# Optimization experiments

Measured on AMD Instinct MI355X. Metric: run time of the kernel, lower is better.

Reference implementation:

```python
import jax, jax.numpy as jnp
import numpy as np

B, L, D = 8192, 2048, 256


def setup_inputs() -> dict:
    key = jax.random.key(0)
    kx, kl = jax.random.split(key)
    x = jax.random.normal(kx, (B, D), dtype=jnp.float32)
    landmarks = jax.random.normal(kl, (L, D), dtype=jnp.float32)
    return {"x": x, "landmarks": landmarks}


def reference(x, landmarks):
    # RBF layer: out[b, l] = exp(-gamma * sum_d (landmarks[l, d] - x[b, d])^2)
    # gamma='auto' -> 1 / n_features (landmarks.shape[1])
    gamma = jnp.float32(1.0 / landmarks.shape[1])
    # avoids materializing the [B, L, D] broadcast-diff intermediate)
    x2 = jnp.sum(x * x, axis=-1, keepdims=True)          # [B, 1]
    l2 = jnp.sum(landmarks * landmarks, axis=-1)         # [L]
    cross = jnp.einsum('bd,ld->bl', x, landmarks)        # [B, L]
    d2 = jnp.maximum(x2 + l2[None, :] - 2.0 * cross, 0.0)
    return jnp.exp(-gamma * d2)
```

## Files before the change

kernel.cpp:

```cpp
#include <hip/hip_runtime.h>


typedef __bf16 bf16x8 __attribute__((ext_vector_type(8)));
typedef float  f32x4  __attribute__((ext_vector_type(4)));

#define B_ROWS 8192
#define L_ROWS 2048
#define K_DIM  256

#define GLD_LDS(g, l) __builtin_amdgcn_global_load_lds(                      \
    (const __attribute__((address_space(1))) void*)(g),                      \
    (__attribute__((address_space(3))) void*)(l), 16, 0, 0)

__device__ __forceinline__ unsigned short f32_to_bf16_rne(float f) {
    union { float f; unsigned int u; } v; v.f = f;
    unsigned int u = v.u;
    unsigned int r = (u + 0x7fffu + ((u >> 16) & 1u)) >> 16;
    return (unsigned short)r;
}

__global__ __launch_bounds__(256) void cvt_rows_kernel(
    const float* __restrict__ in, unsigned short* __restrict__ outb,
    float* __restrict__ sq)
{
    const int lane = threadIdx.x & 63;
    const int row  = blockIdx.x * 4 + (threadIdx.x >> 6);
    const float4 v = ((const float4*)(in + row * K_DIM))[lane];
    ushort4 o;
    o.x = f32_to_bf16_rne(v.x);
    o.y = f32_to_bf16_rne(v.y);
    o.z = f32_to_bf16_rne(v.z);
    o.w = f32_to_bf16_rne(v.w);
    ((ushort4*)(outb + row * K_DIM))[lane] = o;
    float s = v.x*v.x + v.y*v.y + v.z*v.z + v.w*v.w;
    #pragma unroll
    for (int off = 32; off > 0; off >>= 1) s += __shfl_down(s, off, 64);
    if (lane == 0) sq[row] = s;
}

__global__ __launch_bounds__(256) void rbf_gemm_kernel(
    const unsigned short* __restrict__ A,
    const unsigned short* __restrict__ Bm,
    const float* __restrict__ x2,
    const float* __restrict__ l2,
    float* __restrict__ out)
{
    __shared__ unsigned short As[128 * 64];
    __shared__ unsigned short Bs[128 * 64];

    const int tid  = threadIdx.x;
    const int wave = tid >> 6;
    const int lane = tid & 63;
    const int wm = wave >> 1, wn = wave & 1;
    const int bm = blockIdx.x, bn = blockIdx.y;

    f32x4 acc[4][4];
    #pragma unroll
    for (int i = 0; i < 4; ++i)
        #pragma unroll
        for (int j = 0; j < 4; ++j)
            acc[i][j] = (f32x4){0.f, 0.f, 0.f, 0.f};

    const int ldrow = lane >> 3;
    const int ldcol = (lane & 7) * 8;

    const unsigned short* Ab = A  + (bm * 128) * K_DIM;
    const unsigned short* Bb = Bm + (bn * 128) * K_DIM;

    for (int k0 = 0; k0 < K_DIM; k0 += 64) {
        #pragma unroll
        for (int it = 0; it < 4; ++it) {
            const int r = wave * 32 + it * 8;
            GLD_LDS(Ab + (r + ldrow) * K_DIM + k0 + ldcol, &As[r * 64]);
            GLD_LDS(Bb + (r + ldrow) * K_DIM + k0 + ldcol, &Bs[r * 64]);
        }
        __syncthreads();

        #pragma unroll
        for (int kk = 0; kk < 64; kk += 32) {
            const int ko = kk + (lane >> 4) * 8;
            bf16x8 af[4], bfr[4];
            #pragma unroll
            for (int t = 0; t < 4; ++t) {
                af[t]  = *(const bf16x8*)&As[(wm*64 + t*16 + (lane & 15)) * 64 + ko];
                bfr[t] = *(const bf16x8*)&Bs[(wn*64 + t*16 + (lane & 15)) * 64 + ko];
            }
            #pragma unroll
            for (int mt = 0; mt < 4; ++mt)
                #pragma unroll
                for (int nt = 0; nt < 4; ++nt)
                    acc[mt][nt] = __builtin_amdgcn_mfma_f32_16x16x32_bf16(
                        af[mt], bfr[nt], acc[mt][nt], 0, 0, 0);
        }
        __syncthreads();
    }

    const float gamma = 1.0f / 256.0f;
    const int col0 = bn * 128 + wn * 64 + (lane & 15);
    const int row0 = bm * 128 + wm * 64 + (lane >> 4) * 4;
    #pragma unroll
    for (int mt = 0; mt < 4; ++mt) {
        const int rb = row0 + mt * 16;
        float xv[4];
        #pragma unroll
        for (int r = 0; r < 4; ++r) xv[r] = x2[rb + r];
        #pragma unroll
        for (int nt = 0; nt < 4; ++nt) {
            const int c  = col0 + nt * 16;
            const float lv = l2[c];
            #pragma unroll
            for (int r = 0; r < 4; ++r) {
                float d2 = fmaxf(xv[r] + lv - 2.0f * acc[mt][nt][r], 0.0f);
                out[(rb + r) * L_ROWS + c] = __expf(-gamma * d2);
            }
        }
    }
}

extern "C" void kernel_launch(void* const* d_in, const int* in_sizes, int n_in,
                              void* d_out, int out_size, void* d_ws, size_t ws_size,
                              hipStream_t stream) {
    const float* x  = (const float*)d_in[0];
    const float* lm = (const float*)d_in[1];
    float* out = (float*)d_out;

    char* ws = (char*)d_ws;
    unsigned short* xb = (unsigned short*)ws;
    unsigned short* lb = (unsigned short*)(ws + (size_t)B_ROWS*K_DIM*2);
    float* x2 = (float*)(ws + (size_t)B_ROWS*K_DIM*2 + (size_t)L_ROWS*K_DIM*2);
    float* l2 = x2 + B_ROWS;

    cvt_rows_kernel<<<B_ROWS/4, 256, 0, stream>>>(x, xb, x2);
    cvt_rows_kernel<<<L_ROWS/4, 256, 0, stream>>>(lm, lb, l2);
    rbf_gemm_kernel<<<dim3(B_ROWS/128, L_ROWS/128), 256, 0, stream>>>(xb, lb, x2, l2, out);
}
```

Measured before the change: 96.52 us.

## Swap GEMM operand roles, XOR-swizzle LDS, vectorize nontemporal stores, merge conversion kernels

The two bf16 conversion launches are merged into one, and -gamma is folded into the precomputed row norms. The GEMM now treats landmarks as the M operand and x as N, so each lane's four accumulator values land on four consecutive output columns. The epilogue can then write them as one 16-byte nontemporal store with a single FMA and exp per element. LDS tiles get an XOR swizzle on the 16-byte blocks to reduce bank conflicts in the fragment reads. The risk is store coalescing: a wavefront's 16-byte stores now spread across 16 different output rows.

```diff
diff --git a/kernel.cpp b/kernel.cpp
--- a/kernel.cpp
+++ b/kernel.cpp
@@ -7,6 +7,7 @@
 #define B_ROWS 8192
 #define L_ROWS 2048
 #define K_DIM  256
+#define NEG_GAMMA (-1.0f / 256.0f)
 
 #define GLD_LDS(g, l) __builtin_amdgcn_global_load_lds(                      \
     (const __attribute__((address_space(1))) void*)(g),                      \
@@ -15,34 +16,41 @@
 __device__ __forceinline__ unsigned short f32_to_bf16_rne(float f) {
     union { float f; unsigned int u; } v; v.f = f;
     unsigned int u = v.u;
-    unsigned int r = (u + 0x7fffu + ((u >> 16) & 1u)) >> 16;
-    return (unsigned short)r;
+    return (unsigned short)((u + 0x7fffu + ((u >> 16) & 1u)) >> 16);
 }
 
 __global__ __launch_bounds__(256) void cvt_rows_kernel(
-    const float* __restrict__ in, unsigned short* __restrict__ outb,
-    float* __restrict__ sq)
+    const float* __restrict__ x, const float* __restrict__ lm,
+    unsigned short* __restrict__ xb, unsigned short* __restrict__ lb,
+    float* __restrict__ gx2, float* __restrict__ gl2)
 {
     const int lane = threadIdx.x & 63;
     const int row  = blockIdx.x * 4 + (threadIdx.x >> 6);
-    const float4 v = ((const float4*)(in + row * K_DIM))[lane];
+    const float* src; unsigned short* dst; float* nrm;
+    if (row < B_ROWS) {
+        src = x + (size_t)row * K_DIM; dst = xb + (size_t)row * K_DIM; nrm = gx2 + row;
+    } else {
+        const int r = row - B_ROWS;
+        src = lm + (size_t)r * K_DIM; dst = lb + (size_t)r * K_DIM; nrm = gl2 + r;
+    }
+    const float4 v = ((const float4*)src)[lane];
     ushort4 o;
     o.x = f32_to_bf16_rne(v.x);
     o.y = f32_to_bf16_rne(v.y);
     o.z = f32_to_bf16_rne(v.z);
     o.w = f32_to_bf16_rne(v.w);
-    ((ushort4*)(outb + row * K_DIM))[lane] = o;
+    ((ushort4*)dst)[lane] = o;
     float s = v.x*v.x + v.y*v.y + v.z*v.z + v.w*v.w;
     #pragma unroll
     for (int off = 32; off > 0; off >>= 1) s += __shfl_down(s, off, 64);
-    if (lane == 0) sq[row] = s;
+    if (lane == 0) nrm[0] = NEG_GAMMA * s;
 }
 
 __global__ __launch_bounds__(256) void rbf_gemm_kernel(
-    const unsigned short* __restrict__ A,
-    const unsigned short* __restrict__ Bm,
-    const float* __restrict__ x2,
-    const float* __restrict__ l2,
+    const unsigned short* __restrict__ Lmat,
+    const unsigned short* __restrict__ Xmat,
+    const float* __restrict__ gl2,
+    const float* __restrict__ gx2,
     float* __restrict__ out)
 {
     __shared__ unsigned short As[128 * 64];
@@ -52,7 +60,8 @@
     const int wave = tid >> 6;
     const int lane = tid & 63;
     const int wm = wave >> 1, wn = wave & 1;
-    const int bm = blockIdx.x, bn = blockIdx.y;
+    const int bn = blockIdx.x;
+    const int bm = blockIdx.y;
 
     f32x4 acc[4][4];
     #pragma unroll
@@ -61,29 +70,33 @@
         for (int j = 0; j < 4; ++j)
             acc[i][j] = (f32x4){0.f, 0.f, 0.f, 0.f};
 
-    const int ldrow = lane >> 3;
-    const int ldcol = (lane & 7) * 8;
+    const int lrow = lane >> 3;
+    const int lblk = (lane & 7) ^ lrow;
 
-    const unsigned short* Ab = A  + (bm * 128) * K_DIM;
-    const unsigned short* Bb = Bm + (bn * 128) * K_DIM;
+    const unsigned short* Ab = Lmat + (size_t)(bm * 128) * K_DIM;
+    const unsigned short* Bb = Xmat + (size_t)(bn * 128) * K_DIM;
+
+    const int rlo = lane & 15;
+    const int q   = lane >> 4;
 
     for (int k0 = 0; k0 < K_DIM; k0 += 64) {
         #pragma unroll
         for (int it = 0; it < 4; ++it) {
             const int r = wave * 32 + it * 8;
-            GLD_LDS(Ab + (r + ldrow) * K_DIM + k0 + ldcol, &As[r * 64]);
-            GLD_LDS(Bb + (r + ldrow) * K_DIM + k0 + ldcol, &Bs[r * 64]);
+            GLD_LDS(Ab + (size_t)(r + lrow) * K_DIM + k0 + lblk * 8, &As[r * 64]);
+            GLD_LDS(Bb + (size_t)(r + lrow) * K_DIM + k0 + lblk * 8, &Bs[r * 64]);
         }
         __syncthreads();
 
         #pragma unroll
         for (int kk = 0; kk < 64; kk += 32) {
-            const int ko = kk + (lane >> 4) * 8;
+            const int kb = (kk >> 3) + q;
+            const int pb = (kb ^ (rlo & 7)) * 8;
             bf16x8 af[4], bfr[4];
             #pragma unroll
             for (int t = 0; t < 4; ++t) {
-                af[t]  = *(const bf16x8*)&As[(wm*64 + t*16 + (lane & 15)) * 64 + ko];
-                bfr[t] = *(const bf16x8*)&Bs[(wn*64 + t*16 + (lane & 15)) * 64 + ko];
+                af[t]  = *(const bf16x8*)&As[(wm*64 + t*16 + rlo) * 64 + pb];
+                bfr[t] = *(const bf16x8*)&Bs[(wn*64 + t*16 + rlo) * 64 + pb];
             }
             #pragma unroll
             for (int mt = 0; mt < 4; ++mt)
@@ -95,24 +108,24 @@
         __syncthreads();
     }
 
-    const float gamma = 1.0f / 256.0f;
-    const int col0 = bn * 128 + wn * 64 + (lane & 15);
-    const int row0 = bm * 128 + wm * 64 + (lane >> 4) * 4;
+    const float twog = 2.0f / 256.0f;
+    const int b0 = bn * 128 + wn * 64 + rlo;
+    const int l0 = bm * 128 + wm * 64 + q * 4;
     #pragma unroll
-    for (int mt = 0; mt < 4; ++mt) {
-        const int rb = row0 + mt * 16;
-        float xv[4];
+    for (int nt = 0; nt < 4; ++nt) {
+        const int b = b0 + nt * 16;
+        const float gx = gx2[b];
+        float* orow = out + (size_t)b * L_ROWS;
         #pragma unroll
-        for (int r = 0; r < 4; ++r) xv[r] = x2[rb + r];
-        #pragma unroll
-        for (int nt = 0; nt < 4; ++nt) {
-            const int c  = col0 + nt * 16;
-            const float lv = l2[c];
-            #pragma unroll
-            for (int r = 0; r < 4; ++r) {
-                float d2 = fmaxf(xv[r] + lv - 2.0f * acc[mt][nt][r], 0.0f);
-                out[(rb + r) * L_ROWS + c] = __expf(-gamma * d2);
-            }
+        for (int mt = 0; mt < 4; ++mt) {
+            const int l = l0 + mt * 16;
+            const float4 gl = *(const float4*)&gl2[l];
+            f32x4 o;
+            o[0] = __expf(fminf(fmaf(twog, acc[mt][nt][0], gx + gl.x), 0.f));
+            o[1] = __expf(fminf(fmaf(twog, acc[mt][nt][1], gx + gl.y), 0.f));
+            o[2] = __expf(fminf(fmaf(twog, acc[mt][nt][2], gx + gl.z), 0.f));
+            o[3] = __expf(fminf(fmaf(twog, acc[mt][nt][3], gx + gl.w), 0.f));
+            __builtin_nontemporal_store(o, (f32x4*)&orow[l]);
         }
     }
 }
@@ -127,10 +140,9 @@
     char* ws = (char*)d_ws;
     unsigned short* xb = (unsigned short*)ws;
     unsigned short* lb = (unsigned short*)(ws + (size_t)B_ROWS*K_DIM*2);
-    float* x2 = (float*)(ws + (size_t)B_ROWS*K_DIM*2 + (size_t)L_ROWS*K_DIM*2);
-    float* l2 = x2 + B_ROWS;
+    float* gx2 = (float*)(ws + (size_t)B_ROWS*K_DIM*2 + (size_t)L_ROWS*K_DIM*2);
+    float* gl2 = gx2 + B_ROWS;
 
-    cvt_rows_kernel<<<B_ROWS/4, 256, 0, stream>>>(x, xb, x2);
-    cvt_rows_kernel<<<L_ROWS/4, 256, 0, stream>>>(lm, lb, l2);
-    rbf_gemm_kernel<<<dim3(B_ROWS/128, L_ROWS/128), 256, 0, stream>>>(xb, lb, x2, l2, out);
+    cvt_rows_kernel<<<(B_ROWS + L_ROWS)/4, 256, 0, stream>>>(x, lm, xb, lb, gx2, gl2);
+    rbf_gemm_kernel<<<dim3(B_ROWS/128, L_ROWS/128), 256, 0, stream>>>(lb, xb, gl2, gx2, out);
 }
```

After: 98.11 us, median of 2. About the same (+1.6%).
